# Performance work log

Measured on AMD Instinct MI355X. Metric: run time of the kernel, lower is better.

## Reference

```python
import jax, jax.numpy as jnp
import numpy as np

EPS = 1e-5
NUM_GROUPS = 32


def group_norm(x, scale, bias):
    # x: [B, C, H, W], 32 groups, normalized over (C/G, H, W)
    B, C, H, W = x.shape
    G = NUM_GROUPS
    xg = x.reshape(B, G, C // G, H, W)
    mean = xg.mean(axis=(2, 3, 4), keepdims=True)
    var = xg.var(axis=(2, 3, 4), keepdims=True)
    xg = (xg - mean) * jax.lax.rsqrt(var + EPS)
    x = xg.reshape(B, C, H, W)
    return x * scale[None, :, None, None] + bias[None, :, None, None]


def setup_inputs() -> dict:
    key = jax.random.key(0)
    ks = jax.random.split(key, 6)
    B, C, H, W = 32, 512, 32, 32
    std = 1.0 / np.sqrt(C)
    return {
        "x": jax.random.normal(ks[0], (B, C, H, W), dtype=jnp.float32),
        "gn_scale": jnp.ones((C,), dtype=jnp.float32),
        "gn_bias": jnp.zeros((C,), dtype=jnp.float32),
        "wq": jax.random.normal(ks[1], (C, C), dtype=jnp.float32) * std,
        "bq": jnp.zeros((C,), dtype=jnp.float32),
        "wk": jax.random.normal(ks[2], (C, C), dtype=jnp.float32) * std,
        "bk": jnp.zeros((C,), dtype=jnp.float32),
        "wv": jax.random.normal(ks[3], (C, C), dtype=jnp.float32) * std,
        "bv": jnp.zeros((C,), dtype=jnp.float32),
        "wo": jax.random.normal(ks[4], (C, C), dtype=jnp.float32) * std,
        "bo": jnp.zeros((C,), dtype=jnp.float32),
    }


def reference(x, gn_scale, gn_bias, wq, bq, wk, bk, wv, bv, wo, bo):
    B, C, H, W = x.shape
    h = group_norm(x, gn_scale, gn_bias)
    # 1x1 convs == per-pixel matmuls; flatten spatial to tokens: [B, HW, C]
    ht = h.reshape(B, C, H * W).transpose(0, 2, 1)
    q = jnp.einsum('bnc,oc->bno', ht, wq) + bq  # [B, HW, C]
    k = jnp.einsum('bnc,oc->bno', ht, wk) + bk
    v = jnp.einsum('bnc,oc->bno', ht, wv) + bv
    scale = 1.0 / jnp.sqrt(jnp.asarray(C, x.dtype))
    w = jnp.einsum('bnc,bmc->bnm', q, k) * scale  # [B, HW, HW]
    w = jax.nn.softmax(w, axis=-1)
    a = jnp.einsum('bnm,bmc->bnc', w, v)  # [B, HW, C]
    out = jnp.einsum('bnc,oc->bno', a, wo) + bo
    out = out.transpose(0, 2, 1).reshape(B, C, H, W)
    return x + out
```

## Files before the change

kernel.cpp:

```cpp
#include <hip/hip_runtime.h>
#include <stdint.h>

typedef unsigned short u16;
typedef __attribute__((ext_vector_type(8))) short short8;
typedef __attribute__((ext_vector_type(4))) float f32x4;

#define NTOK 1024
#define CDIM 512
#define NG 32

#define GLOAD_LDS16(gptr, lptr)                                                              \
  __builtin_amdgcn_global_load_lds((const __attribute__((address_space(1))) unsigned int*)(gptr), \
                                   (__attribute__((address_space(3))) unsigned int*)(lptr), 16, 0, 0)

__device__ __forceinline__ u16 f2bf(float f) {
  union { float f; uint32_t u; } v; v.f = f;
  uint32_t r = v.u + 0x7fffu + ((v.u >> 16) & 1u);
  return (u16)(r >> 16);
}

__device__ __forceinline__ float bf2f(u16 b) {
  union { uint32_t u; float f; } v; v.u = ((uint32_t)b) << 16;
  return v.f;
}

__global__ __launch_bounds__(256) void wconv(const float* __restrict__ wq, const float* __restrict__ wk,
                                             const float* __restrict__ wv, const float* __restrict__ wo,
                                             const float* __restrict__ bq, const float* __restrict__ bk,
                                             u16* __restrict__ out, float* __restrict__ bqk) {
  int i = blockIdx.x * 256 + threadIdx.x;
  out[i]          = f2bf(wq[i]);
  out[262144 + i] = f2bf(wk[i]);
  out[524288 + i] = f2bf(wv[i]);
  out[786432 + i] = f2bf(wo[i]);
  if (i < 512) bqk[i] = bq[i];
  else if (i < 1024) bqk[i] = bk[i - 512];
}

__global__ __launch_bounds__(256) void gn_stats(const float* __restrict__ x,
                                                float* __restrict__ mean_o, float* __restrict__ rstd_o) {
  int bg = blockIdx.x;
  const float4* base = (const float4*)(x + (size_t)bg * 16384);
  float s = 0.f, ss = 0.f;
  for (int i = threadIdx.x; i < 4096; i += 256) {
    float4 v = base[i];
    s  += v.x + v.y + v.z + v.w;
    ss += v.x * v.x + v.y * v.y + v.z * v.z + v.w * v.w;
  }
#pragma unroll
  for (int d = 1; d < 64; d <<= 1) { s += __shfl_xor(s, d); ss += __shfl_xor(ss, d); }
  __shared__ float as[4], as2[4];
  int w = threadIdx.x >> 6;
  if ((threadIdx.x & 63) == 0) { as[w] = s; as2[w] = ss; }
  __syncthreads();
  if (threadIdx.x == 0) {
    float S = as[0] + as[1] + as[2] + as[3];
    float SS = as2[0] + as2[1] + as2[2] + as2[3];
    float m = S * (1.f / 16384.f);
    float var = SS * (1.f / 16384.f) - m * m;
    mean_o[bg] = m;
    rstd_o[bg] = rsqrtf(var + 1e-5f);
  }
}

__global__ __launch_bounds__(256) void gn_apply(const float* __restrict__ x,
                                                const float* __restrict__ mean_, const float* __restrict__ rstd_,
                                                const float* __restrict__ gsc, const float* __restrict__ gbi,
                                                u16* __restrict__ h) {
  int n0 = blockIdx.x * 64, c0 = blockIdx.y * 64, b = blockIdx.z;
  __shared__ u16 t[64][65];
  int tid = threadIdx.x;
  int nl4 = (tid & 15) * 4;
  int clb = tid >> 4;
#pragma unroll
  for (int p = 0; p < 4; ++p) {
    int cl = p * 16 + clb;
    int c = c0 + cl;
    int g = c >> 4;
    float m = mean_[b * NG + g], rs = rstd_[b * NG + g];
    float sc = gsc[c] * rs, bi = gbi[c] - m * sc;
    float4 v = *(const float4*)(x + ((size_t)b * CDIM + c) * NTOK + n0 + nl4);
    t[cl][nl4 + 0] = f2bf(v.x * sc + bi);
    t[cl][nl4 + 1] = f2bf(v.y * sc + bi);
    t[cl][nl4 + 2] = f2bf(v.z * sc + bi);
    t[cl][nl4 + 3] = f2bf(v.w * sc + bi);
  }
  __syncthreads();
  int nl = tid >> 3;
  int cc = (tid & 7) * 8;
#pragma unroll
  for (int p = 0; p < 2; ++p) {
    int n = nl + p * 32;
    short8 o;
#pragma unroll
    for (int i = 0; i < 8; ++i) o[i] = (short)t[cc + i][n];
    *(short8*)(h + (size_t)(b * NTOK + n0 + n) * CDIM + c0 + cc) = o;
  }
}

template <int MODE>
__device__ __forceinline__ void gemm_body(const u16* __restrict__ A, const u16* __restrict__ B,
                                          const float* __restrict__ bias, u16* __restrict__ outb,
                                          float* __restrict__ outf, const float* __restrict__ resid,
                                          int Ka, int Kb, int nkt,
                                          size_t strideA, size_t strideB, int batch0) {
  int nx = gridDim.x, ny = gridDim.y;
  int nwg = nx * ny * gridDim.z;
  int id = blockIdx.x + nx * (blockIdx.y + ny * blockIdx.z);
  int cpx = nwg >> 3;
  int sw = (id & 7) * cpx + (id >> 3);
  int bx = sw % nx; int t_ = sw / nx;
  int by = t_ % ny; int z = t_ / ny;

  const u16* Amat = A + (size_t)z * strideA;
  const u16* Bmat = B + (size_t)z * strideB;
  int n0 = bx * 256, m0 = by * 256;
  __shared__ u16 As[2][16384];
  __shared__ u16 Bs[2][16384];
  int tid = threadIdx.x;
  int l = tid & 63, wid = tid >> 6;
  int lr = l & 15, lh = l >> 4;
  int wm = (wid >> 2) * 128;
  int wn = (wid & 3) * 64;

  f32x4 acc[8][4];
#pragma unroll
  for (int i = 0; i < 8; ++i)
#pragma unroll
    for (int j = 0; j < 4; ++j) acc[i][j] = (f32x4){0.f, 0.f, 0.f, 0.f};

  short8 af[4][2];
  short8 bf01[2][2];
  short8 bf23[2][2];

  int sr = tid >> 3, sc = tid & 7;
  int sg = (sc ^ (sr & 7)) << 3;
  const u16* Ag0 = Amat + (size_t)(m0 + sr) * Ka + sg;
  const u16* Ag1 = Ag0 + (size_t)64 * Ka;
  const u16* Bg0 = Bmat + (size_t)(n0 + sr) * Kb + sg;
  const u16* Bg1 = Bg0 + (size_t)64 * Kb;
  size_t hA = (size_t)128 * Ka, hB = (size_t)128 * Kb;
  u16* Al0 = &As[0][sr * 64 + sc * 8];
  u16* Bl0 = &Bs[0][sr * 64 + sc * 8];

#define STAGE_A(bufsel, ktv, half)                                        \
  {                                                                       \
    size_t go_ = (size_t)(ktv) * 64 + ((half) ? hA : (size_t)0);          \
    u16* ld_ = Al0 + (bufsel) * 16384 + (half) * 8192;                    \
    GLOAD_LDS16(Ag0 + go_, ld_);                                          \
    GLOAD_LDS16(Ag1 + go_, ld_ + 4096);                                   \
  }
#define STAGE_B(bufsel, ktv, half)                                        \
  {                                                                       \
    size_t go_ = (size_t)(ktv) * 64 + ((half) ? hB : (size_t)0);          \
    u16* ld_ = Bl0 + (bufsel) * 16384 + (half) * 8192;                    \
    GLOAD_LDS16(Bg0 + go_, ld_);                                          \
    GLOAD_LDS16(Bg1 + go_, ld_ + 4096);                                   \
  }

#define READ_AF(ihalf, bufsel)                                                        \
  _Pragma("unroll") for (int i_ = 0; i_ < 4; ++i_) {                                  \
    int row_ = wm + (ihalf) * 64 + i_ * 16 + lr;                                      \
    const u16* p_ = &As[bufsel][row_ * 64];                                           \
    _Pragma("unroll") for (int ks_ = 0; ks_ < 2; ++ks_)                               \
      af[i_][ks_] = *(const short8*)(p_ + (((ks_ * 4 + lh) ^ (row_ & 7)) << 3));      \
  }

#define READ_BF(dst, jbase, bufsel)                                                   \
  _Pragma("unroll") for (int j_ = 0; j_ < 2; ++j_) {                                  \
    int row_ = wn + ((jbase) + j_) * 16 + lr;                                         \
    const u16* p_ = &Bs[bufsel][row_ * 64];                                           \
    _Pragma("unroll") for (int ks_ = 0; ks_ < 2; ++ks_)                               \
      dst[j_][ks_] = *(const short8*)(p_ + (((ks_ * 4 + lh) ^ (row_ & 7)) << 3));     \
  }

#define MFMA_Q(ihalf, jbase, bsrc)                                                    \
  _Pragma("unroll") for (int ks_ = 0; ks_ < 2; ++ks_)                                 \
    _Pragma("unroll") for (int i_ = 0; i_ < 4; ++i_)                                  \
      _Pragma("unroll") for (int j_ = 0; j_ < 2; ++j_)                                \
        acc[(ihalf) * 4 + i_][(jbase) + j_] = __builtin_amdgcn_mfma_f32_16x16x32_bf16( \
            af[i_][ks_], bsrc[j_][ks_], acc[(ihalf) * 4 + i_][(jbase) + j_], 0, 0, 0);

#define PBAR() __builtin_amdgcn_s_barrier()

#define PHASES(BC, BN, GI, DOHI, DOLO)                                    \
  {                                                                       \
    int g1_ = (GI) + 1, g2_ = (GI) + 2;                                   \
                                           \
    READ_AF(0, BC);                                                       \
    READ_BF(bf01, 0, BC);                                                 \
    if (DOHI) { STAGE_A(BN, g1_, 1); }                                    \
    PBAR();                                                               \
    __builtin_amdgcn_s_setprio(1);                                        \
    MFMA_Q(0, 0, bf01);                                                   \
    __builtin_amdgcn_s_setprio(0);                                        \
    PBAR();                                                               \
                                           \
    READ_BF(bf23, 2, BC);                                                 \
    if (DOHI) { STAGE_B(BN, g1_, 1); }                                    \
    PBAR();                                                               \
    __builtin_amdgcn_s_setprio(1);                                        \
    MFMA_Q(0, 2, bf23);                                                   \
    __builtin_amdgcn_s_setprio(0);                                        \
    PBAR();                                                               \
     \
    READ_AF(1, BC);                                                       \
    if (DOLO) { STAGE_B(BC, g2_, 0); }                                    \
    PBAR();                                                               \
    __builtin_amdgcn_s_setprio(1);                                        \
    MFMA_Q(1, 2, bf23);                                                   \
    __builtin_amdgcn_s_setprio(0);                                        \
    PBAR();                                                               \
     \
    if (DOLO) { STAGE_A(BC, g2_, 0); }                                    \
    PBAR();                                                               \
    __builtin_amdgcn_s_setprio(1);                                        \
    MFMA_Q(1, 0, bf01);                                                   \
    __builtin_amdgcn_s_setprio(0);                                        \
    if (DOLO) { asm volatile("s_waitcnt vmcnt(4)"); }                     \
    else      { asm volatile("s_waitcnt vmcnt(0)"); }                     \
    __builtin_amdgcn_sched_barrier(0);                                    \
    PBAR();                                                               \
  }

  int k1 = (1 < nkt) ? 1 : 0;
  STAGE_B(0, 0, 0);
  STAGE_A(0, 0, 0);
  STAGE_A(0, 0, 1);
  STAGE_B(0, 0, 1);
  STAGE_B(1, k1, 0);
  STAGE_A(1, k1, 0);
  asm volatile("s_waitcnt vmcnt(4)");
  __builtin_amdgcn_sched_barrier(0);
  PBAR();

  for (int kt = 0; kt < nkt; kt += 2) {
    int more = (kt + 2 < nkt) ? 1 : 0;
    PHASES(0, 1, kt, 1, more);
    PHASES(1, 0, kt + 1, more, more);
  }

#pragma unroll
  for (int i = 0; i < 8; ++i)
#pragma unroll
    for (int j = 0; j < 4; ++j)
#pragma unroll
      for (int r = 0; r < 4; ++r) {
        int gr = m0 + wm + i * 16 + lh * 4 + r;
        int gc = n0 + wn + j * 16 + lr;
        float v = acc[i][j][r];
        if (MODE == 0) {
          v += bias[gc];
          outb[(size_t)gr * 1024 + gc] = f2bf(v);
        } else if (MODE == 1 || MODE == 2) {
          v += bias[gr];
          int bt = gc >> 10, nn = gc & 1023;
          size_t addr = ((size_t)bt * 512 + gr) * 1024 + nn;
          if (MODE == 1) outb[addr] = f2bf(v);
          else outf[addr] = v + resid[addr];
        } else if (MODE == 3) {
          outb[((size_t)z * 1024 + gr) * 1024 + gc] = f2bf(v);
        } else {
          outb[((size_t)((batch0 + z) * 1024 + gr)) * 512 + gc] = f2bf(v);
        }
      }
#undef STAGE_A
#undef STAGE_B
#undef READ_AF
#undef READ_BF
#undef MFMA_Q
#undef PBAR
#undef PHASES
}

__global__ __launch_bounds__(512, 2) void gemm_qk(const u16* A, const u16* B, const float* bias,
                                                  u16* outb, float* outf, const float* resid,
                                                  int Ka, int Kb, int nkt, size_t sA, size_t sB, int b0) {
  gemm_body<0>(A, B, bias, outb, outf, resid, Ka, Kb, nkt, sA, sB, b0);
}
__global__ __launch_bounds__(512, 2) void gemm_v(const u16* A, const u16* B, const float* bias,
                                                 u16* outb, float* outf, const float* resid,
                                                 int Ka, int Kb, int nkt, size_t sA, size_t sB, int b0) {
  gemm_body<1>(A, B, bias, outb, outf, resid, Ka, Kb, nkt, sA, sB, b0);
}
__global__ __launch_bounds__(512, 2) void gemm_o(const u16* A, const u16* B, const float* bias,
                                                 u16* outb, float* outf, const float* resid,
                                                 int Ka, int Kb, int nkt, size_t sA, size_t sB, int b0) {
  gemm_body<2>(A, B, bias, outb, outf, resid, Ka, Kb, nkt, sA, sB, b0);
}
__global__ __launch_bounds__(512, 2) void gemm_s(const u16* A, const u16* B, const float* bias,
                                                 u16* outb, float* outf, const float* resid,
                                                 int Ka, int Kb, int nkt, size_t sA, size_t sB, int b0) {
  gemm_body<3>(A, B, bias, outb, outf, resid, Ka, Kb, nkt, sA, sB, b0);
}
__global__ __launch_bounds__(512, 2) void gemm_pv(const u16* A, const u16* B, const float* bias,
                                                  u16* outb, float* outf, const float* resid,
                                                  int Ka, int Kb, int nkt, size_t sA, size_t sB, int b0) {
  gemm_body<4>(A, B, bias, outb, outf, resid, Ka, Kb, nkt, sA, sB, b0);
}

__global__ __launch_bounds__(256) void softmax_rows(u16* __restrict__ S) {
  const float scale = 0.04419417382415922f;
  int row = blockIdx.x * 4 + (threadIdx.x >> 6);
  int l = threadIdx.x & 63;
  u16* Sr = S + (size_t)row * 1024;
  short8 a = *(const short8*)(Sr + l * 8);
  short8 b = *(const short8*)(Sr + 512 + l * 8);
  float f[16];
#pragma unroll
  for (int i = 0; i < 8; ++i) { f[i] = bf2f((u16)a[i]); f[8 + i] = bf2f((u16)b[i]); }
  float mx = f[0];
#pragma unroll
  for (int i = 1; i < 16; ++i) mx = fmaxf(mx, f[i]);
#pragma unroll
  for (int d = 1; d < 64; d <<= 1) mx = fmaxf(mx, __shfl_xor(mx, d));
  float s = 0.f;
#pragma unroll
  for (int i = 0; i < 16; ++i) { f[i] = __expf((f[i] - mx) * scale); s += f[i]; }
#pragma unroll
  for (int d = 1; d < 64; d <<= 1) s += __shfl_xor(s, d);
  float inv = 1.f / s;
  short8 oa, ob;
#pragma unroll
  for (int i = 0; i < 8; ++i) { oa[i] = (short)f2bf(f[i] * inv); ob[i] = (short)f2bf(f[8 + i] * inv); }
  *(short8*)(Sr + l * 8) = oa;
  *(short8*)(Sr + 512 + l * 8) = ob;
}

extern "C" void kernel_launch(void* const* d_in, const int* in_sizes, int n_in,
                              void* d_out, int out_size, void* d_ws, size_t ws_size,
                              hipStream_t stream) {
  const float* x   = (const float*)d_in[0];
  const float* gsc = (const float*)d_in[1];
  const float* gbi = (const float*)d_in[2];
  const float* wq  = (const float*)d_in[3];
  const float* bq  = (const float*)d_in[4];
  const float* wk  = (const float*)d_in[5];
  const float* bk  = (const float*)d_in[6];
  const float* wv  = (const float*)d_in[7];
  const float* bv  = (const float*)d_in[8];
  const float* wo  = (const float*)d_in[9];
  const float* bo  = (const float*)d_in[10];

  char* ws = (char*)d_ws;
  u16* wbf = (u16*)ws;
  float* bqk = (float*)(ws + (2ull << 20));
  float* mean_ = (float*)(ws + (2ull << 20) + 65536);
  float* rstd_ = mean_ + 1024;
  u16* h   = (u16*)(ws + (4ull << 20));
  u16* qk  = (u16*)(ws + (36ull << 20));
  u16* vm  = (u16*)(ws + (100ull << 20));
  u16* S   = (u16*)(ws + (132ull << 20));
  u16* am  = h;
  float* out = (float*)d_out;

  size_t sbytes = ws_size > (132ull << 20) ? ws_size - (132ull << 20) : 0;
  int CB = 1;
  while (CB < 32 && (size_t)(CB * 2) * (2ull << 20) <= sbytes) CB *= 2;

  wconv<<<1024, 256, 0, stream>>>(wq, wk, wv, wo, bq, bk, wbf, bqk);
  gn_stats<<<1024, 256, 0, stream>>>(x, mean_, rstd_);
  gn_apply<<<dim3(16, 8, 32), 256, 0, stream>>>(x, mean_, rstd_, gsc, gbi, h);
  gemm_qk<<<dim3(4, 128), 512, 0, stream>>>(h, wbf, bqk, qk, nullptr, nullptr,
                                            512, 512, 8, 0, 0, 0);
  gemm_v<<<dim3(128, 2), 512, 0, stream>>>(wbf + 524288, h, bv, vm, nullptr, nullptr,
                                           512, 512, 8, 0, 0, 0);
  for (int c0 = 0; c0 < 32; c0 += CB) {
    gemm_s<<<dim3(4, 4, CB), 512, 0, stream>>>(qk + (size_t)c0 * 1048576, qk + 512 + (size_t)c0 * 1048576,
                                               nullptr, S, nullptr, nullptr,
                                               1024, 1024, 8, 1048576, 1048576, 0);
    softmax_rows<<<CB * 256, 256, 0, stream>>>(S);
    gemm_pv<<<dim3(2, 4, CB), 512, 0, stream>>>(S, vm + (size_t)c0 * 524288,
                                                nullptr, am, nullptr, nullptr,
                                                1024, 1024, 16, 1048576, 524288, c0);
  }
  gemm_o<<<dim3(128, 2), 512, 0, stream>>>(wbf + 786432, am, bo, nullptr, out, x,
                                           512, 512, 8, 0, 0, 0);
}
```

Measured before the change: 261.1 us.

## Fuse Q/K/V projection GEMMs and stage all GEMM epilogues through LDS

```diff
diff --git a/kernel.cpp b/kernel.cpp
--- a/kernel.cpp
+++ b/kernel.cpp
@@ -3,6 +3,7 @@
 
 typedef unsigned short u16;
 typedef __attribute__((ext_vector_type(8))) short short8;
+typedef __attribute__((ext_vector_type(4))) short s16x4;
 typedef __attribute__((ext_vector_type(4))) float f32x4;
 
 #define NTOK 1024
@@ -27,14 +28,16 @@
 __global__ __launch_bounds__(256) void wconv(const float* __restrict__ wq, const float* __restrict__ wk,
                                              const float* __restrict__ wv, const float* __restrict__ wo,
                                              const float* __restrict__ bq, const float* __restrict__ bk,
-                                             u16* __restrict__ out, float* __restrict__ bqk) {
+                                             const float* __restrict__ bv,
+                                             u16* __restrict__ out, float* __restrict__ bqkv) {
   int i = blockIdx.x * 256 + threadIdx.x;
   out[i]          = f2bf(wq[i]);
   out[262144 + i] = f2bf(wk[i]);
   out[524288 + i] = f2bf(wv[i]);
   out[786432 + i] = f2bf(wo[i]);
-  if (i < 512) bqk[i] = bq[i];
-  else if (i < 1024) bqk[i] = bk[i - 512];
+  if (i < 512) bqkv[i] = bq[i];
+  else if (i < 1024) bqkv[i] = bk[i - 512];
+  else if (i < 1536) bqkv[i] = bv[i - 1024];
 }
 
 __global__ __launch_bounds__(256) void gn_stats(const float* __restrict__ x,
@@ -101,6 +104,7 @@
 template <int MODE>
 __device__ __forceinline__ void gemm_body(const u16* __restrict__ A, const u16* __restrict__ B,
                                           const float* __restrict__ bias, u16* __restrict__ outb,
+                                          u16* __restrict__ outb2,
                                           float* __restrict__ outf, const float* __restrict__ resid,
                                           int Ka, int Kb, int nkt,
                                           size_t strideA, size_t strideB, int batch0) {
@@ -115,8 +119,7 @@
   const u16* Amat = A + (size_t)z * strideA;
   const u16* Bmat = B + (size_t)z * strideB;
   int n0 = bx * 256, m0 = by * 256;
-  __shared__ u16 As[2][16384];
-  __shared__ u16 Bs[2][16384];
+  __shared__ __align__(16) u16 SH[65536];
   int tid = threadIdx.x;
   int l = tid & 63, wid = tid >> 6;
   int lr = l & 15, lh = l >> 4;
@@ -140,8 +143,8 @@
   const u16* Bg0 = Bmat + (size_t)(n0 + sr) * Kb + sg;
   const u16* Bg1 = Bg0 + (size_t)64 * Kb;
   size_t hA = (size_t)128 * Ka, hB = (size_t)128 * Kb;
-  u16* Al0 = &As[0][sr * 64 + sc * 8];
-  u16* Bl0 = &Bs[0][sr * 64 + sc * 8];
+  u16* Al0 = SH + sr * 64 + sc * 8;
+  u16* Bl0 = SH + 32768 + sr * 64 + sc * 8;
 
 #define STAGE_A(bufsel, ktv, half)                                        \
   {                                                                       \
@@ -161,7 +164,7 @@
 #define READ_AF(ihalf, bufsel)                                                        \
   _Pragma("unroll") for (int i_ = 0; i_ < 4; ++i_) {                                  \
     int row_ = wm + (ihalf) * 64 + i_ * 16 + lr;                                      \
-    const u16* p_ = &As[bufsel][row_ * 64];                                           \
+    const u16* p_ = SH + (bufsel) * 16384 + row_ * 64;                                \
     _Pragma("unroll") for (int ks_ = 0; ks_ < 2; ++ks_)                               \
       af[i_][ks_] = *(const short8*)(p_ + (((ks_ * 4 + lh) ^ (row_ & 7)) << 3));      \
   }
@@ -169,7 +172,7 @@
 #define READ_BF(dst, jbase, bufsel)                                                   \
   _Pragma("unroll") for (int j_ = 0; j_ < 2; ++j_) {                                  \
     int row_ = wn + ((jbase) + j_) * 16 + lr;                                         \
-    const u16* p_ = &Bs[bufsel][row_ * 64];                                           \
+    const u16* p_ = SH + 32768 + (bufsel) * 16384 + row_ * 64;                        \
     _Pragma("unroll") for (int ks_ = 0; ks_ < 2; ++ks_)                               \
       dst[j_][ks_] = *(const short8*)(p_ + (((ks_ * 4 + lh) ^ (row_ & 7)) << 3));     \
   }
@@ -240,30 +243,130 @@
     PHASES(1, 0, kt + 1, more, more);
   }
 
-#pragma unroll
-  for (int i = 0; i < 8; ++i)
-#pragma unroll
-    for (int j = 0; j < 4; ++j)
-#pragma unroll
-      for (int r = 0; r < 4; ++r) {
-        int gr = m0 + wm + i * 16 + lh * 4 + r;
-        int gc = n0 + wn + j * 16 + lr;
-        float v = acc[i][j][r];
-        if (MODE == 0) {
-          v += bias[gc];
-          outb[(size_t)gr * 1024 + gc] = f2bf(v);
-        } else if (MODE == 1 || MODE == 2) {
-          v += bias[gr];
-          int bt = gc >> 10, nn = gc & 1023;
-          size_t addr = ((size_t)bt * 512 + gr) * 1024 + nn;
-          if (MODE == 1) outb[addr] = f2bf(v);
-          else outf[addr] = v + resid[addr];
-        } else if (MODE == 3) {
-          outb[((size_t)z * 1024 + gr) * 1024 + gc] = f2bf(v);
-        } else {
-          outb[((size_t)((batch0 + z) * 1024 + gr)) * 512 + gc] = f2bf(v);
+  __syncthreads();
+  const int gr0 = m0 + wm, gc0 = n0 + wn;
+  u16* eb = SH + wid * 4352;
+
+  if constexpr (MODE == 5) {
+    float bj[4];
+#pragma unroll
+    for (int j = 0; j < 4; ++j) bj[j] = bias[gc0 + j * 16 + lr];
+    if (n0 < 1024) {
+#pragma unroll
+      for (int pass = 0; pass < 2; ++pass) {
+#pragma unroll
+        for (int i2 = 0; i2 < 4; ++i2)
+#pragma unroll
+          for (int j = 0; j < 4; ++j)
+#pragma unroll
+            for (int r = 0; r < 4; ++r)
+              eb[(i2 * 16 + lh * 4 + r) * 68 + j * 16 + lr] =
+                  f2bf(acc[pass * 4 + i2][j][r] + bj[j]);
+        asm volatile("s_waitcnt lgkmcnt(0)");
+        __builtin_amdgcn_sched_barrier(0);
+#pragma unroll
+        for (int t = 0; t < 8; ++t) {
+          int row = t * 8 + (l >> 3), c8 = (l & 7) * 8;
+          s16x4 lo = *(const s16x4*)(eb + row * 68 + c8);
+          s16x4 hi = *(const s16x4*)(eb + row * 68 + c8 + 4);
+          short8 o;
+          o[0] = lo[0]; o[1] = lo[1]; o[2] = lo[2]; o[3] = lo[3];
+          o[4] = hi[0]; o[5] = hi[1]; o[6] = hi[2]; o[7] = hi[3];
+          *(short8*)(outb + (size_t)(gr0 + pass * 64 + row) * 1024 + gc0 + c8) = o;
         }
+        asm volatile("s_waitcnt lgkmcnt(0)");
+        __builtin_amdgcn_sched_barrier(0);
       }
+    } else {
+      int ch0 = gc0 - 1024;
+      int bt = m0 >> 10, tok0 = (m0 & 1023) + wm;
+#pragma unroll
+      for (int pass = 0; pass < 2; ++pass) {
+#pragma unroll
+        for (int i2 = 0; i2 < 4; ++i2)
+#pragma unroll
+          for (int j = 0; j < 4; ++j) {
+            s16x4 w;
+#pragma unroll
+            for (int r = 0; r < 4; ++r)
+              w[r] = (short)f2bf(acc[pass * 4 + i2][j][r] + bj[j]);
+            *(s16x4*)(eb + (j * 16 + lr) * 68 + i2 * 16 + lh * 4) = w;
+          }
+        asm volatile("s_waitcnt lgkmcnt(0)");
+        __builtin_amdgcn_sched_barrier(0);
+#pragma unroll
+        for (int t = 0; t < 8; ++t) {
+          int row = t * 8 + (l >> 3), c8 = (l & 7) * 8;
+          s16x4 lo = *(const s16x4*)(eb + row * 68 + c8);
+          s16x4 hi = *(const s16x4*)(eb + row * 68 + c8 + 4);
+          short8 o;
+          o[0] = lo[0]; o[1] = lo[1]; o[2] = lo[2]; o[3] = lo[3];
+          o[4] = hi[0]; o[5] = hi[1]; o[6] = hi[2]; o[7] = hi[3];
+          *(short8*)(outb2 + (size_t)(bt * 512 + ch0 + row) * 1024 + tok0 + pass * 64 + c8) = o;
+        }
+        asm volatile("s_waitcnt lgkmcnt(0)");
+        __builtin_amdgcn_sched_barrier(0);
+      }
+    }
+  } else if constexpr (MODE == 3 || MODE == 4) {
+    u16* obase = (MODE == 3) ? (outb + (size_t)z * 1048576)
+                             : (outb + (size_t)(batch0 + z) * 524288);
+    const int LD = (MODE == 3) ? 1024 : 512;
+#pragma unroll
+    for (int pass = 0; pass < 2; ++pass) {
+#pragma unroll
+      for (int i2 = 0; i2 < 4; ++i2)
+#pragma unroll
+        for (int j = 0; j < 4; ++j)
+#pragma unroll
+          for (int r = 0; r < 4; ++r)
+            eb[(i2 * 16 + lh * 4 + r) * 68 + j * 16 + lr] =
+                f2bf(acc[pass * 4 + i2][j][r]);
+      asm volatile("s_waitcnt lgkmcnt(0)");
+      __builtin_amdgcn_sched_barrier(0);
+#pragma unroll
+      for (int t = 0; t < 8; ++t) {
+        int row = t * 8 + (l >> 3), c8 = (l & 7) * 8;
+        s16x4 lo = *(const s16x4*)(eb + row * 68 + c8);
+        s16x4 hi = *(const s16x4*)(eb + row * 68 + c8 + 4);
+        short8 o;
+        o[0] = lo[0]; o[1] = lo[1]; o[2] = lo[2]; o[3] = lo[3];
+        o[4] = hi[0]; o[5] = hi[1]; o[6] = hi[2]; o[7] = hi[3];
+        *(short8*)(obase + (size_t)(gr0 + pass * 64 + row) * LD + gc0 + c8) = o;
+      }
+      asm volatile("s_waitcnt lgkmcnt(0)");
+      __builtin_amdgcn_sched_barrier(0);
+    }
+  } else {
+    float* ebf = (float*)SH + wid * 2176;
+    int bt = n0 >> 10, nn0 = (n0 & 1023) + wn;
+#pragma unroll
+    for (int pass = 0; pass < 4; ++pass) {
+#pragma unroll
+      for (int i2 = 0; i2 < 2; ++i2)
+#pragma unroll
+        for (int r = 0; r < 4; ++r) {
+          float bv = bias[gr0 + pass * 32 + i2 * 16 + lh * 4 + r];
+#pragma unroll
+          for (int j = 0; j < 4; ++j)
+            ebf[(i2 * 16 + lh * 4 + r) * 68 + j * 16 + lr] =
+                acc[pass * 2 + i2][j][r] + bv;
+        }
+      asm volatile("s_waitcnt lgkmcnt(0)");
+      __builtin_amdgcn_sched_barrier(0);
+#pragma unroll
+      for (int t = 0; t < 8; ++t) {
+        int row = t * 4 + (l >> 4), c4 = (l & 15) * 4;
+        float4 vv = *(const float4*)(ebf + row * 68 + c4);
+        size_t addr = ((size_t)bt * 512 + gr0 + pass * 32 + row) * 1024 + nn0 + c4;
+        const float4 rr = *(const float4*)(resid + addr);
+        vv.x += rr.x; vv.y += rr.y; vv.z += rr.z; vv.w += rr.w;
+        *(float4*)(outf + addr) = vv;
+      }
+      asm volatile("s_waitcnt lgkmcnt(0)");
+      __builtin_amdgcn_sched_barrier(0);
+    }
+  }
 #undef STAGE_A
 #undef STAGE_B
 #undef READ_AF
@@ -273,30 +376,25 @@
 #undef PHASES
 }
 
-__global__ __launch_bounds__(512, 2) void gemm_qk(const u16* A, const u16* B, const float* bias,
-                                                  u16* outb, float* outf, const float* resid,
+__global__ __launch_bounds__(512, 2) void gemm_qkv(const u16* A, const u16* B, const float* bias,
+                                                   u16* outb, u16* outb2, float* outf, const float* resid,
+                                                   int Ka, int Kb, int nkt, size_t sA, size_t sB, int b0) {
+  gemm_body<5>(A, B, bias, outb, outb2, outf, resid, Ka, Kb, nkt, sA, sB, b0);
+}
+__global__ __launch_bounds__(512, 2) void gemm_o(const u16* A, const u16* B, const float* bias,
+                                                 u16* outb, u16* outb2, float* outf, const float* resid,
+                                                 int Ka, int Kb, int nkt, size_t sA, size_t sB, int b0) {
+  gemm_body<2>(A, B, bias, outb, outb2, outf, resid, Ka, Kb, nkt, sA, sB, b0);
+}
+__global__ __launch_bounds__(512, 2) void gemm_s(const u16* A, const u16* B, const float* bias,
+                                                 u16* outb, u16* outb2, float* outf, const float* resid,
+                                                 int Ka, int Kb, int nkt, size_t sA, size_t sB, int b0) {
+  gemm_body<3>(A, B, bias, outb, outb2, outf, resid, Ka, Kb, nkt, sA, sB, b0);
+}
+__global__ __launch_bounds__(512, 2) void gemm_pv(const u16* A, const u16* B, const float* bias,
+                                                  u16* outb, u16* outb2, float* outf, const float* resid,
                                                   int Ka, int Kb, int nkt, size_t sA, size_t sB, int b0) {
-  gemm_body<0>(A, B, bias, outb, outf, resid, Ka, Kb, nkt, sA, sB, b0);
-}
-__global__ __launch_bounds__(512, 2) void gemm_v(const u16* A, const u16* B, const float* bias,
-                                                 u16* outb, float* outf, const float* resid,
-                                                 int Ka, int Kb, int nkt, size_t sA, size_t sB, int b0) {
-  gemm_body<1>(A, B, bias, outb, outf, resid, Ka, Kb, nkt, sA, sB, b0);
-}
-__global__ __launch_bounds__(512, 2) void gemm_o(const u16* A, const u16* B, const float* bias,
-                                                 u16* outb, float* outf, const float* resid,
-                                                 int Ka, int Kb, int nkt, size_t sA, size_t sB, int b0) {
-  gemm_body<2>(A, B, bias, outb, outf, resid, Ka, Kb, nkt, sA, sB, b0);
-}
-__global__ __launch_bounds__(512, 2) void gemm_s(const u16* A, const u16* B, const float* bias,
-                                                 u16* outb, float* outf, const float* resid,
-                                                 int Ka, int Kb, int nkt, size_t sA, size_t sB, int b0) {
-  gemm_body<3>(A, B, bias, outb, outf, resid, Ka, Kb, nkt, sA, sB, b0);
-}
-__global__ __launch_bounds__(512, 2) void gemm_pv(const u16* A, const u16* B, const float* bias,
-                                                  u16* outb, float* outf, const float* resid,
-                                                  int Ka, int Kb, int nkt, size_t sA, size_t sB, int b0) {
-  gemm_body<4>(A, B, bias, outb, outf, resid, Ka, Kb, nkt, sA, sB, b0);
+  gemm_body<4>(A, B, bias, outb, outb2, outf, resid, Ka, Kb, nkt, sA, sB, b0);
 }
 
 __global__ __launch_bounds__(256) void softmax_rows(u16* __restrict__ S) {
@@ -344,7 +442,7 @@
 
   char* ws = (char*)d_ws;
   u16* wbf = (u16*)ws;
-  float* bqk = (float*)(ws + (2ull << 20));
+  float* bqkv = (float*)(ws + (2ull << 20));
   float* mean_ = (float*)(ws + (2ull << 20) + 65536);
   float* rstd_ = mean_ + 1024;
   u16* h   = (u16*)(ws + (4ull << 20));
@@ -358,22 +456,20 @@
   int CB = 1;
   while (CB < 32 && (size_t)(CB * 2) * (2ull << 20) <= sbytes) CB *= 2;
 
-  wconv<<<1024, 256, 0, stream>>>(wq, wk, wv, wo, bq, bk, wbf, bqk);
+  wconv<<<1024, 256, 0, stream>>>(wq, wk, wv, wo, bq, bk, bv, wbf, bqkv);
   gn_stats<<<1024, 256, 0, stream>>>(x, mean_, rstd_);
   gn_apply<<<dim3(16, 8, 32), 256, 0, stream>>>(x, mean_, rstd_, gsc, gbi, h);
-  gemm_qk<<<dim3(4, 128), 512, 0, stream>>>(h, wbf, bqk, qk, nullptr, nullptr,
-                                            512, 512, 8, 0, 0, 0);
-  gemm_v<<<dim3(128, 2), 512, 0, stream>>>(wbf + 524288, h, bv, vm, nullptr, nullptr,
-                                           512, 512, 8, 0, 0, 0);
+  gemm_qkv<<<dim3(6, 128), 512, 0, stream>>>(h, wbf, bqkv, qk, vm, nullptr, nullptr,
+                                             512, 512, 8, 0, 0, 0);
   for (int c0 = 0; c0 < 32; c0 += CB) {
     gemm_s<<<dim3(4, 4, CB), 512, 0, stream>>>(qk + (size_t)c0 * 1048576, qk + 512 + (size_t)c0 * 1048576,
-                                               nullptr, S, nullptr, nullptr,
+                                               nullptr, S, nullptr, nullptr, nullptr,
                                                1024, 1024, 8, 1048576, 1048576, 0);
     softmax_rows<<<CB * 256, 256, 0, stream>>>(S);
     gemm_pv<<<dim3(2, 4, CB), 512, 0, stream>>>(S, vm + (size_t)c0 * 524288,
-                                                nullptr, am, nullptr, nullptr,
+                                                nullptr, am, nullptr, nullptr, nullptr,
                                                 1024, 1024, 16, 1048576, 524288, c0);
   }
-  gemm_o<<<dim3(128, 2), 512, 0, stream>>>(wbf + 786432, am, bo, nullptr, out, x,
+  gemm_o<<<dim3(128, 2), 512, 0, stream>>>(wbf + 786432, am, bo, nullptr, nullptr, out, x,
                                            512, 512, 8, 0, 0, 0);
 }
```

New measurement: 241.8 us. -7.4%, faster.
